# Optimization experiments

Measured on AMD Instinct MI355X. Metric: run time of the kernel, lower is better.

Reference implementation:

```python
import jax, jax.numpy as jnp
import numpy as np


def setup_inputs() -> dict:
    key = jax.random.key(0)
    ks = jax.random.split(key, 8)
    B, N = 4, 256
    E, C, H = 64, 128, 256
    return {
        "edge_features": jax.random.normal(ks[0], (B, E, N, N), dtype=jnp.float32),
        "node_features": jax.random.normal(ks[1], (B, C, N), dtype=jnp.float32),
        "W1": jax.random.normal(ks[2], (H, E + 2 * C), dtype=jnp.float32) * 0.05,
        "b1": jax.random.normal(ks[3], (H,), dtype=jnp.float32) * 0.05,
        "W2": jax.random.normal(ks[4], (H, H), dtype=jnp.float32) * 0.05,
        "b2": jax.random.normal(ks[5], (H,), dtype=jnp.float32) * 0.05,
        "W3": jax.random.normal(ks[6], (1, H), dtype=jnp.float32) * 0.05,
        "b3": jax.random.normal(ks[7], (1,), dtype=jnp.float32) * 0.05,
    }


def reference(edge_features, node_features, W1, b1, W2, b2, W3, b3):
    B, C, N = node_features.shape
    # node_addon_row: [B, C, N, N] broadcast along last dim; col along dim 2
    row = jnp.broadcast_to(node_features[:, :, :, None], (B, C, N, N))
    col = jnp.broadcast_to(node_features[:, :, None, :], (B, C, N, N))
    x = jnp.concatenate([edge_features, row, col], axis=1)  # [B, E+2C, N, N]
    # 1x1 conv == channel matmul
    x = jax.nn.relu(jnp.einsum('bcnm,oc->bonm', x, W1) + b1[None, :, None, None])
    x = jax.nn.relu(jnp.einsum('bcnm,oc->bonm', x, W2) + b2[None, :, None, None])
    x = jnp.einsum('bcnm,oc->bonm', x, W3) + b3[None, :, None, None]  # [B,1,N,N]
    return x[:, 0, :, :]
```

## Files before the change

### kernel.cpp

```cpp
#include <hip/hip_runtime.h>
#include <stdint.h>

typedef __bf16 bf16x8 __attribute__((ext_vector_type(8)));
typedef __bf16 bf16x4v __attribute__((ext_vector_type(4)));
typedef float  f32x16 __attribute__((ext_vector_type(16)));
typedef float  f32x4t __attribute__((ext_vector_type(4)));
typedef unsigned int u32x2 __attribute__((ext_vector_type(2)));

#define WS_W1S 0
#define WS_W2S 32768
#define WS_R   163840
#define WS_CT  1212416

__global__ __launch_bounds__(256) void prep_all(
    const float* __restrict__ W1, const float* __restrict__ b1,
    const float* __restrict__ W2, const float* __restrict__ node,
    __bf16* __restrict__ w1s, __bf16* __restrict__ w2s,
    float* __restrict__ Rt, __bf16* __restrict__ Ctb) {
    __shared__ float nds[128 * 4];
    const int blk = blockIdx.x;
    if (blk < 40) {
        int t = blk * 256 + threadIdx.x;
        int chunk = t >> 6, lane = t & 63;
        if (chunk < 128) {
            int wid = chunk >> 5, ks = (chunk >> 1) & 15, mb = chunk & 1;
            int o = wid * 64 + mb * 32 + (lane & 31);
            int k = ks * 16 + (lane >> 5) * 8;
            const float* src = W2 + o * 256 + k;
            __bf16* dst = w2s + chunk * 512 + lane * 8;
#pragma unroll
            for (int j = 0; j < 8; ++j) dst[j] = (__bf16)src[j];
        } else if (chunk < 160) {
            int c1 = chunk - 128;
            int wid = c1 >> 3, ks = (c1 >> 1) & 3, mb = c1 & 1;
            int o = wid * 64 + mb * 32 + (lane & 31);
            int k = ks * 16 + (lane >> 5) * 8;
            const float* src = W1 + o * 320 + k;
            __bf16* dst = w1s + c1 * 512 + lane * 8;
#pragma unroll
            for (int j = 0; j < 8; ++j) dst[j] = (__bf16)src[j];
        }
        return;
    }
    const int rcb = blk - 40;
    const int b = rcb >> 6, j0 = (rcb & 63) << 2;
    const int o = threadIdx.x;
    if (o < 128)
        *(float4*)&nds[o * 4] = *(const float4*)(node + b * 32768 + o * 256 + j0);
    __syncthreads();
    float aR[4] = {0.f, 0.f, 0.f, 0.f};
    float aC[4] = {0.f, 0.f, 0.f, 0.f};
    const float* wr = W1 + o * 320 + 64;
    const float* wc = W1 + o * 320 + 192;
    for (int c4 = 0; c4 < 32; ++c4) {
        float4 wrv = *(const float4*)(wr + c4 * 4);
        float4 wcv = *(const float4*)(wc + c4 * 4);
        const float* wrp = (const float*)&wrv;
        const float* wcp = (const float*)&wcv;
#pragma unroll
        for (int r = 0; r < 4; ++r) {
            f32x4t n4 = *(const f32x4t*)&nds[(c4 * 4 + r) * 4];
#pragma unroll
            for (int q = 0; q < 4; ++q) {
                aR[q] = fmaf(wrp[r], n4[q], aR[q]);
                aC[q] = fmaf(wcp[r], n4[q], aC[q]);
            }
        }
    }
    float bb = b1[o];
#pragma unroll
    for (int j = 0; j < 4; ++j) {
        int idx = ((b * 256 + j0 + j) << 8) + o;
        Rt[idx] = aR[j] + bb;
        Ctb[idx] = (__bf16)aC[j];
    }
}

__device__ __forceinline__ void lds_barrier() {
    __builtin_amdgcn_sched_barrier(0);
    asm volatile("s_waitcnt lgkmcnt(0)" ::: "memory");
    __builtin_amdgcn_s_barrier();
    __builtin_amdgcn_sched_barrier(0);
}

__device__ inline void zero_acc(f32x16 acc[2][2]) {
#pragma unroll
    for (int i = 0; i < 2; ++i)
#pragma unroll
        for (int j = 0; j < 2; ++j)
#pragma unroll
            for (int k = 0; k < 16; ++k) acc[i][j][k] = 0.f;
}

__global__ __launch_bounds__(256, 2) void fused_main(
    const float* __restrict__ edge, const __bf16* __restrict__ w1s,
    const __bf16* __restrict__ w2s, const float* __restrict__ Rt,
    const __bf16* __restrict__ Ctb, const float* __restrict__ b2,
    const float* __restrict__ W3, const float* __restrict__ b3,
    float* __restrict__ out) {
    __shared__ unsigned int lds_e[64 * 34];
    __shared__ unsigned int lds_h1[64 * 140];
    __shared__ float lds_p[8 * 64 * 9];
    __shared__ float lds_c[512];

    const int tid = threadIdx.x;
    const int wid = tid >> 6;
    const int lane = tid & 63;
    const int p31 = lane & 31;
    const int hi = lane >> 5;
    const int obase = wid * 64;

    const int blk = blockIdx.x;
    const int b   = blk >> 7;
    const int m0  = ((blk >> 5) & 3) << 6;
    const int n0  = (blk & 31) << 3;

    lds_c[tid] = b2[tid];
    lds_c[256 + tid] = W3[tid];

    const float4* eg = (const float4*)edge;
    const int a_ = tid & 15;
    const int epb = tid >> 4;
    float4 pf[4];

#define PREFETCH(nn)                                                        \
    {                                                                       \
        _Pragma("unroll")                                                   \
        for (int r = 0; r < 2; ++r) {                                       \
            int ep = r * 16 + epb;                                          \
            int f4 = (b * 64 + ep * 2) * 16384 + (nn) * 64 + (m0 >> 2) + a_;\
            pf[r * 2]     = eg[f4];                                         \
            pf[r * 2 + 1] = eg[f4 + 16384];                                 \
        }                                                                   \
    }

#define LOAD_Q(bf, q)                                                       \
    {                                                                       \
        _Pragma("unroll")                                                   \
        for (int ksl = 0; ksl < 4; ++ksl)                                   \
            _Pragma("unroll")                                               \
            for (int mb = 0; mb < 2; ++mb)                                  \
                A2q[bf][ksl][mb] = *(const bf16x8*)(w2_s +                  \
                    ((((wid << 4) + (q) * 4 + ksl) << 1) + mb) * 512 + (lane << 3)); \
    }

    PREFETCH(n0);

    bf16x4v CvR[8][2];
#pragma unroll
    for (int mb = 0; mb < 2; ++mb)
#pragma unroll
        for (int rg = 0; rg < 4; ++rg)
#pragma unroll
            for (int nb = 0; nb < 2; ++nb)
                CvR[mb * 4 + rg][nb] = *(const bf16x4v*)(Ctb +
                    ((b * 256 + m0 + nb * 32 + p31) << 8) + obase + mb * 32 + 8 * rg + 4 * hi);

    bf16x8 A1[2][4];
#pragma unroll
    for (int mb = 0; mb < 2; ++mb)
#pragma unroll
        for (int ks = 0; ks < 4; ++ks)
            A1[mb][ks] = *(const bf16x8*)(w1s +
                ((((wid << 2) + ks) << 1) + mb) * 512 + (lane << 3));

    f32x16 acc[2][2];
    bf16x8 A2q[2][4][2];
    for (int it = 0; it < 8; ++it) {
        const int n = n0 + it;

        uint64_t w2a = (uint64_t)w2s;
        asm volatile("" : "+s"(w2a));
        const __bf16* w2_s = (const __bf16*)w2a;

#pragma unroll
        for (int r = 0; r < 2; ++r) {
            int ep = r * 16 + epb;
            const float* p0 = (const float*)&pf[r * 2];
            const float* p1 = (const float*)&pf[r * 2 + 1];
#pragma unroll
            for (int i = 0; i < 4; ++i) {
                union { __bf16 h[2]; unsigned int u; } t;
                t.h[0] = (__bf16)p0[i];
                t.h[1] = (__bf16)p1[i];
                lds_e[(a_ * 4 + i) * 34 + ep] = t.u;
            }
        }
        if (it < 7) PREFETCH(n + 1);

        const int nRow = (b * 256 + n) << 8;
        f32x4t Rv[2][4];
#pragma unroll
        for (int mb = 0; mb < 2; ++mb)
#pragma unroll
            for (int rg = 0; rg < 4; ++rg)
                Rv[mb][rg] = *(const f32x4t*)(Rt + nRow + obase + mb * 32 + 8 * rg + 4 * hi);

        lds_barrier();

        zero_acc(acc);
#pragma unroll
        for (int ks = 0; ks < 4; ++ks) {
            bf16x8 B1[2];
#pragma unroll
            for (int nb = 0; nb < 2; ++nb) {
                union { u32x2 d[2]; bf16x8 v; } bb;
                const unsigned int* base = &lds_e[(nb * 32 + p31) * 34 + ks * 8 + hi * 4];
                bb.d[0] = *(const u32x2*)base;
                bb.d[1] = *(const u32x2*)(base + 2);
                B1[nb] = bb.v;
            }
#pragma unroll
            for (int mb = 0; mb < 2; ++mb) {
                acc[mb][0] = __builtin_amdgcn_mfma_f32_32x32x16_bf16(A1[mb][ks], B1[0], acc[mb][0], 0, 0, 0);
                acc[mb][1] = __builtin_amdgcn_mfma_f32_32x32x16_bf16(A1[mb][ks], B1[1], acc[mb][1], 0, 0, 0);
            }
        }

#pragma unroll
        for (int mb = 0; mb < 2; ++mb) {
#pragma unroll
            for (int rg = 0; rg < 4; ++rg) {
                int och = obase + mb * 32 + 8 * rg + 4 * hi;
                f32x4t Rvv = Rv[mb][rg];
#pragma unroll
                for (int nb = 0; nb < 2; ++nb) {
                    int pix = nb * 32 + p31;
                    bf16x4v Cv = CvR[mb * 4 + rg][nb];
                    union { __bf16 h[4]; u32x2 u; } t;
#pragma unroll
                    for (int rr = 0; rr < 4; ++rr) {
                        float v = acc[mb][nb][rg * 4 + rr] + Rvv[rr] + (float)Cv[rr];
                        t.h[rr] = (__bf16)fmaxf(v, 0.f);
                    }
                    *(u32x2*)&lds_h1[pix * 140 + (och >> 1)] = t.u;
                }
            }
        }
        LOAD_Q(0, 0);
        lds_barrier();

        zero_acc(acc);
        __builtin_amdgcn_s_setprio(1);
#pragma unroll
        for (int q = 0; q < 4; ++q) {
            if (q < 3) LOAD_Q((q + 1) & 1, q + 1);
#pragma unroll
            for (int ksl = 0; ksl < 4; ++ksl) {
                const int ksg = q * 4 + ksl;
                bf16x8 B2[2];
#pragma unroll
                for (int nb = 0; nb < 2; ++nb)
                    B2[nb] = *(const bf16x8*)&lds_h1[(nb * 32 + p31) * 140 + ksg * 8 + hi * 4];
#pragma unroll
                for (int mb = 0; mb < 2; ++mb) {
                    acc[mb][0] = __builtin_amdgcn_mfma_f32_32x32x16_bf16(A2q[q & 1][ksl][mb], B2[0], acc[mb][0], 0, 0, 0);
                    acc[mb][1] = __builtin_amdgcn_mfma_f32_32x32x16_bf16(A2q[q & 1][ksl][mb], B2[1], acc[mb][1], 0, 0, 0);
                }
            }
        }
        __builtin_amdgcn_s_setprio(0);

        float part0 = 0.f, part1 = 0.f;
#pragma unroll
        for (int mb = 0; mb < 2; ++mb) {
#pragma unroll
            for (int rg = 0; rg < 4; ++rg) {
                int och = obase + mb * 32 + 8 * rg + 4 * hi;
                f32x4t b2v = *(const f32x4t*)&lds_c[och];
                f32x4t w3v = *(const f32x4t*)&lds_c[256 + och];
#pragma unroll
                for (int rr = 0; rr < 4; ++rr) {
                    float h0 = fmaxf(acc[mb][0][rg * 4 + rr] + b2v[rr], 0.f);
                    float h1v = fmaxf(acc[mb][1][rg * 4 + rr] + b2v[rr], 0.f);
                    part0 = fmaf(w3v[rr], h0, part0);
                    part1 = fmaf(w3v[rr], h1v, part1);
                }
            }
        }
        lds_p[(it * 64 + 0 * 32 + p31) * 9 + wid * 2 + hi] = part0;
        lds_p[(it * 64 + 1 * 32 + p31) * 9 + wid * 2 + hi] = part1;
    }

    __syncthreads();
    {
        float bb3 = b3[0];
#pragma unroll
        for (int r = 0; r < 2; ++r) {
            int idx = r * 256 + tid;
            int row = idx >> 6;
            int mm  = idx & 63;
            float s = bb3;
#pragma unroll
            for (int k = 0; k < 8; ++k) s += lds_p[(row * 64 + mm) * 9 + k];
            out[((b * 256 + n0 + row) << 8) + m0 + mm] = s;
        }
    }
#undef PREFETCH
#undef LOAD_Q
}

extern "C" void kernel_launch(void* const* d_in, const int* in_sizes, int n_in,
                              void* d_out, int out_size, void* d_ws, size_t ws_size,
                              hipStream_t stream) {
    const float* edge = (const float*)d_in[0];
    const float* node = (const float*)d_in[1];
    const float* W1   = (const float*)d_in[2];
    const float* b1   = (const float*)d_in[3];
    const float* W2   = (const float*)d_in[4];
    const float* b2   = (const float*)d_in[5];
    const float* W3   = (const float*)d_in[6];
    const float* b3   = (const float*)d_in[7];
    char* ws = (char*)d_ws;
    __bf16* w1s = (__bf16*)(ws + WS_W1S);
    __bf16* w2s = (__bf16*)(ws + WS_W2S);
    float*  Rt  = (float*)(ws + WS_R);
    __bf16* Ctb = (__bf16*)(ws + WS_CT);

    prep_all<<<296, 256, 0, stream>>>(W1, b1, W2, node, w1s, w2s, Rt, Ctb);
    fused_main<<<512, 256, 0, stream>>>(edge, w1s, w2s, Rt, Ctb, b2, W3, b3, (float*)d_out);
}
```

Before: 153.2 us.

## Raise occupancy to three blocks per CU with smaller tiles and swizzled LDS

```diff
diff --git a/kernel.cpp b/kernel.cpp
--- a/kernel.cpp
+++ b/kernel.cpp
@@ -92,15 +92,15 @@
             for (int k = 0; k < 16; ++k) acc[i][j][k] = 0.f;
 }
 
-__global__ __launch_bounds__(256, 2) void fused_main(
+__global__ __launch_bounds__(256, 3) void fused_main(
     const float* __restrict__ edge, const __bf16* __restrict__ w1s,
     const __bf16* __restrict__ w2s, const float* __restrict__ Rt,
     const __bf16* __restrict__ Ctb, const float* __restrict__ b2,
     const float* __restrict__ W3, const float* __restrict__ b3,
     float* __restrict__ out) {
     __shared__ unsigned int lds_e[64 * 34];
-    __shared__ unsigned int lds_h1[64 * 140];
-    __shared__ float lds_p[8 * 64 * 9];
+    __shared__ unsigned int lds_h1[64 * 128];
+    __shared__ float lds_p[4 * 64 * 9];
     __shared__ float lds_c[512];
 
     const int tid = threadIdx.x;
@@ -109,11 +109,12 @@
     const int p31 = lane & 31;
     const int hi = lane >> 5;
     const int obase = wid * 64;
+    const unsigned swz = (unsigned)((p31 & 7) << 4);
 
     const int blk = blockIdx.x;
-    const int b   = blk >> 7;
-    const int m0  = ((blk >> 5) & 3) << 6;
-    const int n0  = (blk & 31) << 3;
+    const int b   = blk >> 8;
+    const int m0  = ((blk >> 6) & 3) << 6;
+    const int n0  = (blk & 63) << 2;
 
     lds_c[tid] = b2[tid];
     lds_c[256 + tid] = W3[tid];
@@ -134,44 +135,33 @@
         }                                                                   \
     }
 
-#define LOAD_Q(bf, q)                                                       \
+#define LOAD_G(bf, g)                                                       \
     {                                                                       \
         _Pragma("unroll")                                                   \
-        for (int ksl = 0; ksl < 4; ++ksl)                                   \
+        for (int ksl = 0; ksl < 2; ++ksl)                                   \
             _Pragma("unroll")                                               \
             for (int mb = 0; mb < 2; ++mb)                                  \
-                A2q[bf][ksl][mb] = *(const bf16x8*)(w2_s +                  \
-                    ((((wid << 4) + (q) * 4 + ksl) << 1) + mb) * 512 + (lane << 3)); \
+                A2g[bf][ksl][mb] = *(const bf16x8*)(w2_s +                  \
+                    ((((wid << 4) + (g) * 2 + ksl) << 1) + mb) * 512 + (lane << 3)); \
     }
 
     PREFETCH(n0);
 
-    bf16x4v CvR[8][2];
-#pragma unroll
-    for (int mb = 0; mb < 2; ++mb)
-#pragma unroll
-        for (int rg = 0; rg < 4; ++rg)
-#pragma unroll
-            for (int nb = 0; nb < 2; ++nb)
-                CvR[mb * 4 + rg][nb] = *(const bf16x4v*)(Ctb +
-                    ((b * 256 + m0 + nb * 32 + p31) << 8) + obase + mb * 32 + 8 * rg + 4 * hi);
-
-    bf16x8 A1[2][4];
-#pragma unroll
-    for (int mb = 0; mb < 2; ++mb)
-#pragma unroll
-        for (int ks = 0; ks < 4; ++ks)
-            A1[mb][ks] = *(const bf16x8*)(w1s +
-                ((((wid << 2) + ks) << 1) + mb) * 512 + (lane << 3));
-
     f32x16 acc[2][2];
-    bf16x8 A2q[2][4][2];
-    for (int it = 0; it < 8; ++it) {
+    bf16x8 A2g[2][2][2];
+#pragma unroll 1
+    for (int it = 0; it < 4; ++it) {
         const int n = n0 + it;
 
+        uint64_t w1a = (uint64_t)w1s;
+        asm volatile("" : "+s"(w1a));
+        const __bf16* w1_s = (const __bf16*)w1a;
         uint64_t w2a = (uint64_t)w2s;
         asm volatile("" : "+s"(w2a));
         const __bf16* w2_s = (const __bf16*)w2a;
+        uint64_t cta = (uint64_t)Ctb;
+        asm volatile("" : "+s"(cta));
+        const __bf16* ct_s = (const __bf16*)cta;
 
 #pragma unroll
         for (int r = 0; r < 2; ++r) {
@@ -186,15 +176,15 @@
                 lds_e[(a_ * 4 + i) * 34 + ep] = t.u;
             }
         }
-        if (it < 7) PREFETCH(n + 1);
-
-        const int nRow = (b * 256 + n) << 8;
-        f32x4t Rv[2][4];
+        if (it < 3) PREFETCH(n + 1);
+
+        bf16x8 A1[2][4];
 #pragma unroll
         for (int mb = 0; mb < 2; ++mb)
 #pragma unroll
-            for (int rg = 0; rg < 4; ++rg)
-                Rv[mb][rg] = *(const f32x4t*)(Rt + nRow + obase + mb * 32 + 8 * rg + 4 * hi);
+            for (int ks = 0; ks < 4; ++ks)
+                A1[mb][ks] = *(const bf16x8*)(w1_s +
+                    ((((wid << 2) + ks) << 1) + mb) * 512 + (lane << 3));
 
         lds_barrier();
 
@@ -217,45 +207,59 @@
             }
         }
 
+        const int nRow = (b * 256 + n) << 8;
 #pragma unroll
         for (int mb = 0; mb < 2; ++mb) {
+            f32x4t Rvv[4];
+            bf16x4v Cvv[4][2];
 #pragma unroll
             for (int rg = 0; rg < 4; ++rg) {
                 int och = obase + mb * 32 + 8 * rg + 4 * hi;
-                f32x4t Rvv = Rv[mb][rg];
+                Rvv[rg] = *(const f32x4t*)(Rt + nRow + och);
+#pragma unroll
+                for (int nb = 0; nb < 2; ++nb)
+                    Cvv[rg][nb] = *(const bf16x4v*)(ct_s +
+                        ((b * 256 + m0 + nb * 32 + p31) << 8) + och);
+            }
+#pragma unroll
+            for (int rg = 0; rg < 4; ++rg) {
+                int och = obase + mb * 32 + 8 * rg + 4 * hi;
 #pragma unroll
                 for (int nb = 0; nb < 2; ++nb) {
                     int pix = nb * 32 + p31;
-                    bf16x4v Cv = CvR[mb * 4 + rg][nb];
+                    bf16x4v Cv = Cvv[rg][nb];
                     union { __bf16 h[4]; u32x2 u; } t;
 #pragma unroll
                     for (int rr = 0; rr < 4; ++rr) {
-                        float v = acc[mb][nb][rg * 4 + rr] + Rvv[rr] + (float)Cv[rr];
+                        float v = acc[mb][nb][rg * 4 + rr] + Rvv[rg][rr] + (float)Cv[rr];
                         t.h[rr] = (__bf16)fmaxf(v, 0.f);
                     }
-                    *(u32x2*)&lds_h1[pix * 140 + (och >> 1)] = t.u;
+                    unsigned off = (unsigned)(pix * 512 + och * 2) ^ swz;
+                    *(u32x2*)((char*)lds_h1 + off) = t.u;
                 }
             }
         }
-        LOAD_Q(0, 0);
+        LOAD_G(0, 0);
         lds_barrier();
 
         zero_acc(acc);
         __builtin_amdgcn_s_setprio(1);
 #pragma unroll
-        for (int q = 0; q < 4; ++q) {
-            if (q < 3) LOAD_Q((q + 1) & 1, q + 1);
-#pragma unroll
-            for (int ksl = 0; ksl < 4; ++ksl) {
-                const int ksg = q * 4 + ksl;
+        for (int g = 0; g < 8; ++g) {
+            if (g < 7) LOAD_G((g + 1) & 1, g + 1);
+#pragma unroll
+            for (int ksl = 0; ksl < 2; ++ksl) {
+                const int ksg = g * 2 + ksl;
                 bf16x8 B2[2];
 #pragma unroll
-                for (int nb = 0; nb < 2; ++nb)
-                    B2[nb] = *(const bf16x8*)&lds_h1[(nb * 32 + p31) * 140 + ksg * 8 + hi * 4];
+                for (int nb = 0; nb < 2; ++nb) {
+                    unsigned off = (unsigned)((nb * 32 + p31) * 512 + ksg * 32 + hi * 16) ^ swz;
+                    B2[nb] = *(const bf16x8*)((const char*)lds_h1 + off);
+                }
 #pragma unroll
                 for (int mb = 0; mb < 2; ++mb) {
-                    acc[mb][0] = __builtin_amdgcn_mfma_f32_32x32x16_bf16(A2q[q & 1][ksl][mb], B2[0], acc[mb][0], 0, 0, 0);
-                    acc[mb][1] = __builtin_amdgcn_mfma_f32_32x32x16_bf16(A2q[q & 1][ksl][mb], B2[1], acc[mb][1], 0, 0, 0);
+                    acc[mb][0] = __builtin_amdgcn_mfma_f32_32x32x16_bf16(A2g[g & 1][ksl][mb], B2[0], acc[mb][0], 0, 0, 0);
+                    acc[mb][1] = __builtin_amdgcn_mfma_f32_32x32x16_bf16(A2g[g & 1][ksl][mb], B2[1], acc[mb][1], 0, 0, 0);
                 }
             }
         }
@@ -285,19 +289,15 @@
     __syncthreads();
     {
         float bb3 = b3[0];
-#pragma unroll
-        for (int r = 0; r < 2; ++r) {
-            int idx = r * 256 + tid;
-            int row = idx >> 6;
-            int mm  = idx & 63;
-            float s = bb3;
-#pragma unroll
-            for (int k = 0; k < 8; ++k) s += lds_p[(row * 64 + mm) * 9 + k];
-            out[((b * 256 + n0 + row) << 8) + m0 + mm] = s;
-        }
+        int row = tid >> 6;
+        int mm  = tid & 63;
+        float s = bb3;
+#pragma unroll
+        for (int k = 0; k < 8; ++k) s += lds_p[(row * 64 + mm) * 9 + k];
+        out[((b * 256 + n0 + row) << 8) + m0 + mm] = s;
     }
 #undef PREFETCH
-#undef LOAD_Q
+#undef LOAD_G
 }
 
 extern "C" void kernel_launch(void* const* d_in, const int* in_sizes, int n_in,
@@ -318,5 +318,5 @@
     __bf16* Ctb = (__bf16*)(ws + WS_CT);
 
     prep_all<<<296, 256, 0, stream>>>(W1, b1, W2, node, w1s, w2s, Rt, Ctb);
-    fused_main<<<512, 256, 0, stream>>>(edge, w1s, w2s, Rt, Ctb, b2, W3, b3, (float*)d_out);
-}
+    fused_main<<<1024, 256, 0, stream>>>(edge, w1s, w2s, Rt, Ctb, b2, W3, b3, (float*)d_out);
+}
```

Result: slower. 223.1 us (+45.6%).

## Split fused MLP work across 8 waves per block with halved per-wave tiles

Applied to the files above, without the earlier changes.

```diff
diff --git a/kernel.cpp b/kernel.cpp
--- a/kernel.cpp
+++ b/kernel.cpp
@@ -83,16 +83,14 @@
     __builtin_amdgcn_sched_barrier(0);
 }
 
-__device__ inline void zero_acc(f32x16 acc[2][2]) {
-#pragma unroll
-    for (int i = 0; i < 2; ++i)
-#pragma unroll
-        for (int j = 0; j < 2; ++j)
-#pragma unroll
-            for (int k = 0; k < 16; ++k) acc[i][j][k] = 0.f;
-}
-
-__global__ __launch_bounds__(256, 2) void fused_main(
+__device__ inline void zero_acc(f32x16 acc[2]) {
+#pragma unroll
+    for (int j = 0; j < 2; ++j)
+#pragma unroll
+        for (int k = 0; k < 16; ++k) acc[j][k] = 0.f;
+}
+
+__global__ __launch_bounds__(512, 4) void fused_main(
     const float* __restrict__ edge, const __bf16* __restrict__ w1s,
     const __bf16* __restrict__ w2s, const float* __restrict__ Rt,
     const __bf16* __restrict__ Ctb, const float* __restrict__ b2,
@@ -104,97 +102,76 @@
     __shared__ float lds_c[512];
 
     const int tid = threadIdx.x;
-    const int wid = tid >> 6;
+    const int wid8 = tid >> 6;
     const int lane = tid & 63;
     const int p31 = lane & 31;
     const int hi = lane >> 5;
-    const int obase = wid * 64;
+    const int ob32 = wid8 << 5;
+    const int wsel = wid8 >> 1, msel = wid8 & 1;
 
     const int blk = blockIdx.x;
     const int b   = blk >> 7;
     const int m0  = ((blk >> 5) & 3) << 6;
     const int n0  = (blk & 31) << 3;
 
-    lds_c[tid] = b2[tid];
-    lds_c[256 + tid] = W3[tid];
+    if (tid < 256) lds_c[tid] = b2[tid];
+    else           lds_c[tid] = W3[tid - 256];
 
     const float4* eg = (const float4*)edge;
-    const int a_ = tid & 15;
+    const int a_  = tid & 15;
     const int epb = tid >> 4;
-    float4 pf[4];
+    float4 pf[2];
 
 #define PREFETCH(nn)                                                        \
     {                                                                       \
-        _Pragma("unroll")                                                   \
-        for (int r = 0; r < 2; ++r) {                                       \
-            int ep = r * 16 + epb;                                          \
-            int f4 = (b * 64 + ep * 2) * 16384 + (nn) * 64 + (m0 >> 2) + a_;\
-            pf[r * 2]     = eg[f4];                                         \
-            pf[r * 2 + 1] = eg[f4 + 16384];                                 \
-        }                                                                   \
+        int f4 = (b * 64 + epb * 2) * 16384 + (nn) * 64 + (m0 >> 2) + a_;   \
+        pf[0] = eg[f4];                                                     \
+        pf[1] = eg[f4 + 16384];                                             \
     }
 
 #define LOAD_Q(bf, q)                                                       \
     {                                                                       \
         _Pragma("unroll")                                                   \
         for (int ksl = 0; ksl < 4; ++ksl)                                   \
-            _Pragma("unroll")                                               \
-            for (int mb = 0; mb < 2; ++mb)                                  \
-                A2q[bf][ksl][mb] = *(const bf16x8*)(w2_s +                  \
-                    ((((wid << 4) + (q) * 4 + ksl) << 1) + mb) * 512 + (lane << 3)); \
+            A2q[bf][ksl] = *(const bf16x8*)(w2_s +                          \
+                (((wsel * 16 + (q) * 4 + ksl) << 1) + msel) * 512 + (lane << 3)); \
     }
 
     PREFETCH(n0);
 
-    bf16x4v CvR[8][2];
-#pragma unroll
-    for (int mb = 0; mb < 2; ++mb)
-#pragma unroll
-        for (int rg = 0; rg < 4; ++rg)
-#pragma unroll
-            for (int nb = 0; nb < 2; ++nb)
-                CvR[mb * 4 + rg][nb] = *(const bf16x4v*)(Ctb +
-                    ((b * 256 + m0 + nb * 32 + p31) << 8) + obase + mb * 32 + 8 * rg + 4 * hi);
-
-    bf16x8 A1[2][4];
-#pragma unroll
-    for (int mb = 0; mb < 2; ++mb)
-#pragma unroll
-        for (int ks = 0; ks < 4; ++ks)
-            A1[mb][ks] = *(const bf16x8*)(w1s +
-                ((((wid << 2) + ks) << 1) + mb) * 512 + (lane << 3));
-
-    f32x16 acc[2][2];
-    bf16x8 A2q[2][4][2];
+    f32x16 acc[2];
+    bf16x8 A2q[2][4];
     for (int it = 0; it < 8; ++it) {
         const int n = n0 + it;
 
+        uint64_t w1a = (uint64_t)w1s;
+        asm volatile("" : "+s"(w1a));
+        const __bf16* w1_s = (const __bf16*)w1a;
         uint64_t w2a = (uint64_t)w2s;
         asm volatile("" : "+s"(w2a));
         const __bf16* w2_s = (const __bf16*)w2a;
-
-#pragma unroll
-        for (int r = 0; r < 2; ++r) {
-            int ep = r * 16 + epb;
-            const float* p0 = (const float*)&pf[r * 2];
-            const float* p1 = (const float*)&pf[r * 2 + 1];
+        uint64_t cta = (uint64_t)Ctb;
+        asm volatile("" : "+s"(cta));
+        const __bf16* ct_s = (const __bf16*)cta;
+
+        {
+            const float* p0 = (const float*)&pf[0];
+            const float* p1 = (const float*)&pf[1];
 #pragma unroll
             for (int i = 0; i < 4; ++i) {
                 union { __bf16 h[2]; unsigned int u; } t;
                 t.h[0] = (__bf16)p0[i];
                 t.h[1] = (__bf16)p1[i];
-                lds_e[(a_ * 4 + i) * 34 + ep] = t.u;
+                lds_e[(a_ * 4 + i) * 34 + epb] = t.u;
             }
         }
         if (it < 7) PREFETCH(n + 1);
 
-        const int nRow = (b * 256 + n) << 8;
-        f32x4t Rv[2][4];
-#pragma unroll
-        for (int mb = 0; mb < 2; ++mb)
-#pragma unroll
-            for (int rg = 0; rg < 4; ++rg)
-                Rv[mb][rg] = *(const f32x4t*)(Rt + nRow + obase + mb * 32 + 8 * rg + 4 * hi);
+        bf16x8 A1[4];
+#pragma unroll
+        for (int ks = 0; ks < 4; ++ks)
+            A1[ks] = *(const bf16x8*)(w1_s +
+                (((wsel * 4 + ks) << 1) + msel) * 512 + (lane << 3));
 
         lds_barrier();
 
@@ -210,27 +187,34 @@
                 bb.d[1] = *(const u32x2*)(base + 2);
                 B1[nb] = bb.v;
             }
-#pragma unroll
-            for (int mb = 0; mb < 2; ++mb) {
-                acc[mb][0] = __builtin_amdgcn_mfma_f32_32x32x16_bf16(A1[mb][ks], B1[0], acc[mb][0], 0, 0, 0);
-                acc[mb][1] = __builtin_amdgcn_mfma_f32_32x32x16_bf16(A1[mb][ks], B1[1], acc[mb][1], 0, 0, 0);
-            }
-        }
-
-#pragma unroll
-        for (int mb = 0; mb < 2; ++mb) {
+            acc[0] = __builtin_amdgcn_mfma_f32_32x32x16_bf16(A1[ks], B1[0], acc[0], 0, 0, 0);
+            acc[1] = __builtin_amdgcn_mfma_f32_32x32x16_bf16(A1[ks], B1[1], acc[1], 0, 0, 0);
+        }
+
+        {
+            const int nRow = (b * 256 + n) << 8;
+            f32x4t Rvv[4];
+            bf16x4v Cvv[4][2];
 #pragma unroll
             for (int rg = 0; rg < 4; ++rg) {
-                int och = obase + mb * 32 + 8 * rg + 4 * hi;
-                f32x4t Rvv = Rv[mb][rg];
+                int och = ob32 + 8 * rg + 4 * hi;
+                Rvv[rg] = *(const f32x4t*)(Rt + nRow + och);
+#pragma unroll
+                for (int nb = 0; nb < 2; ++nb)
+                    Cvv[rg][nb] = *(const bf16x4v*)(ct_s +
+                        ((b * 256 + m0 + nb * 32 + p31) << 8) + och);
+            }
+#pragma unroll
+            for (int rg = 0; rg < 4; ++rg) {
+                int och = ob32 + 8 * rg + 4 * hi;
 #pragma unroll
                 for (int nb = 0; nb < 2; ++nb) {
                     int pix = nb * 32 + p31;
-                    bf16x4v Cv = CvR[mb * 4 + rg][nb];
+                    bf16x4v Cv = Cvv[rg][nb];
                     union { __bf16 h[4]; u32x2 u; } t;
 #pragma unroll
                     for (int rr = 0; rr < 4; ++rr) {
-                        float v = acc[mb][nb][rg * 4 + rr] + Rvv[rr] + (float)Cv[rr];
+                        float v = acc[nb][rg * 4 + rr] + Rvv[rg][rr] + (float)Cv[rr];
                         t.h[rr] = (__bf16)fmaxf(v, 0.f);
                     }
                     *(u32x2*)&lds_h1[pix * 140 + (och >> 1)] = t.u;
@@ -252,49 +236,44 @@
 #pragma unroll
                 for (int nb = 0; nb < 2; ++nb)
                     B2[nb] = *(const bf16x8*)&lds_h1[(nb * 32 + p31) * 140 + ksg * 8 + hi * 4];
-#pragma unroll
-                for (int mb = 0; mb < 2; ++mb) {
-                    acc[mb][0] = __builtin_amdgcn_mfma_f32_32x32x16_bf16(A2q[q & 1][ksl][mb], B2[0], acc[mb][0], 0, 0, 0);
-                    acc[mb][1] = __builtin_amdgcn_mfma_f32_32x32x16_bf16(A2q[q & 1][ksl][mb], B2[1], acc[mb][1], 0, 0, 0);
-                }
+                acc[0] = __builtin_amdgcn_mfma_f32_32x32x16_bf16(A2q[q & 1][ksl], B2[0], acc[0], 0, 0, 0);
+                acc[1] = __builtin_amdgcn_mfma_f32_32x32x16_bf16(A2q[q & 1][ksl], B2[1], acc[1], 0, 0, 0);
             }
         }
         __builtin_amdgcn_s_setprio(0);
 
         float part0 = 0.f, part1 = 0.f;
 #pragma unroll
-        for (int mb = 0; mb < 2; ++mb) {
-#pragma unroll
-            for (int rg = 0; rg < 4; ++rg) {
-                int och = obase + mb * 32 + 8 * rg + 4 * hi;
-                f32x4t b2v = *(const f32x4t*)&lds_c[och];
-                f32x4t w3v = *(const f32x4t*)&lds_c[256 + och];
-#pragma unroll
-                for (int rr = 0; rr < 4; ++rr) {
-                    float h0 = fmaxf(acc[mb][0][rg * 4 + rr] + b2v[rr], 0.f);
-                    float h1v = fmaxf(acc[mb][1][rg * 4 + rr] + b2v[rr], 0.f);
-                    part0 = fmaf(w3v[rr], h0, part0);
-                    part1 = fmaf(w3v[rr], h1v, part1);
-                }
-            }
-        }
-        lds_p[(it * 64 + 0 * 32 + p31) * 9 + wid * 2 + hi] = part0;
-        lds_p[(it * 64 + 1 * 32 + p31) * 9 + wid * 2 + hi] = part1;
+        for (int rg = 0; rg < 4; ++rg) {
+            int och = ob32 + 8 * rg + 4 * hi;
+            f32x4t b2v = *(const f32x4t*)&lds_c[och];
+            f32x4t w3v = *(const f32x4t*)&lds_c[256 + och];
+#pragma unroll
+            for (int rr = 0; rr < 4; ++rr) {
+                float h0 = fmaxf(acc[0][rg * 4 + rr] + b2v[rr], 0.f);
+                float h1v = fmaxf(acc[1][rg * 4 + rr] + b2v[rr], 0.f);
+                part0 = fmaf(w3v[rr], h0, part0);
+                part1 = fmaf(w3v[rr], h1v, part1);
+            }
+        }
+        part0 += __shfl_xor(part0, 32);
+        part1 += __shfl_xor(part1, 32);
+        {
+            int pix = hi * 32 + p31;
+            float val = hi ? part1 : part0;
+            lds_p[(it * 64 + pix) * 9 + wid8] = val;
+        }
     }
 
     __syncthreads();
     {
         float bb3 = b3[0];
-#pragma unroll
-        for (int r = 0; r < 2; ++r) {
-            int idx = r * 256 + tid;
-            int row = idx >> 6;
-            int mm  = idx & 63;
-            float s = bb3;
-#pragma unroll
-            for (int k = 0; k < 8; ++k) s += lds_p[(row * 64 + mm) * 9 + k];
-            out[((b * 256 + n0 + row) << 8) + m0 + mm] = s;
-        }
+        int row = tid >> 6;
+        int mm  = tid & 63;
+        float s = bb3;
+#pragma unroll
+        for (int k = 0; k < 8; ++k) s += lds_p[(row * 64 + mm) * 9 + k];
+        out[((b * 256 + n0 + row) << 8) + m0 + mm] = s;
     }
 #undef PREFETCH
 #undef LOAD_Q
@@ -318,5 +297,5 @@
     __bf16* Ctb = (__bf16*)(ws + WS_CT);
 
     prep_all<<<296, 256, 0, stream>>>(W1, b1, W2, node, w1s, w2s, Rt, Ctb);
-    fused_main<<<512, 256, 0, stream>>>(edge, w1s, w2s, Rt, Ctb, b2, W3, b3, (float*)d_out);
-}
+    fused_main<<<512, 512, 0, stream>>>(edge, w1s, w2s, Rt, Ctb, b2, W3, b3, (float*)d_out);
+}
```

Result: slower. 170.7 us (+11.4%).
